# Performance work log

Measured on AMD Instinct MI355X. Metric: run time of the kernel, lower is better.

The kernel has to match this reference:

```python
import jax, jax.numpy as jnp
import numpy as np

NORM_EPS = 1e-6

B, C, H, W = 4, 256, 48, 48
CE = 512           # C * expansion_ratio
N_STATE = 16       # Mamba d_state
DT_RANK = 32       # Ce // 16


def setup_inputs() -> dict:
    key = jax.random.key(0)
    ks = jax.random.split(key, 12)
    s = 0.02
    inp = {
        "x": jax.random.normal(ks[0], (B, C, H, W), jnp.float32),
        "norm_w": jnp.ones((C,), jnp.float32),
        "norm_b": jnp.zeros((C,), jnp.float32),
        "w_ex": jax.random.normal(ks[1], (2 * CE, C), jnp.float32) * s,
        "b_ex": jnp.zeros((2 * CE,), jnp.float32),
        "w_proj": jax.random.normal(ks[2], (C, CE), jnp.float32) * s,
        "b_proj": jnp.zeros((C,), jnp.float32),
        "dw_kernel": jax.random.normal(ks[3], (3, 3, 1, CE), jnp.float32) * 0.1,  # HWIO depthwise
        "A_log": jnp.log(jnp.broadcast_to(jnp.arange(1, N_STATE + 1, dtype=jnp.float32), (CE, N_STATE))),
        "D": jnp.ones((CE,), jnp.float32),
        "W_xproj": jax.random.normal(ks[4], (DT_RANK + 2 * N_STATE, CE), jnp.float32) * s,
        "b_xproj": jnp.zeros((DT_RANK + 2 * N_STATE,), jnp.float32),
        "W_dt": jax.random.normal(ks[5], (CE, DT_RANK), jnp.float32) * s,
        "b_dt": jnp.full((CE,), -3.0, jnp.float32),  # softplus -> small positive dt
    }
    return inp


def _forward(x, norm_w, norm_b, w_ex, b_ex, w_proj, b_proj,
             dw_kernel, A_log, D, W_xproj, b_xproj, W_dt, b_dt):
    Bt, Cc, Hh, Ww = x.shape
    Ce = dw_kernel.shape[-1]
    Ns = A_log.shape[1]
    dt_rank = W_dt.shape[1]

    # NCHW -> NHWC, LayerNorm over C
    xp = jnp.transpose(x, (0, 2, 3, 1))
    mu = xp.mean(-1, keepdims=True)
    var = xp.var(-1, keepdims=True)
    xn = (xp - mu) * jax.lax.rsqrt(var + NORM_EPS) * norm_w + norm_b

    # expansion + split
    uv = xn @ w_ex.T + b_ex                       # [B,H,W,2Ce]
    u, v = jnp.split(uv, 2, axis=-1)
    gate = u * jax.nn.sigmoid(-u)                 # r_silu(u)
    g = u * jax.nn.sigmoid(u)                     # SiLU(u)

    # depthwise 3x3 conv (NHWC) + SiLU
    v = jax.lax.conv_general_dilated(
        v, dw_kernel, window_strides=(1, 1), padding='SAME',
        dimension_numbers=('NHWC', 'HWIO', 'NHWC'), feature_group_count=Ce)
    v = v * jax.nn.sigmoid(v)

    gate = v * gate                               # fuse gate before SSM

    # ---- Mamba selective scan over raster-flattened HW sequence ----
    L = Hh * Ww
    vs = v.reshape(Bt, L, Ce)                     # [B,L,Ce]
    dbc = vs @ W_xproj.T + b_xproj                # [B,L,dt_rank+2N]
    dt = dbc[..., :dt_rank]
    Bm = dbc[..., dt_rank:dt_rank + Ns]           # [B,L,N]
    Cm = dbc[..., dt_rank + Ns:]                  # [B,L,N]
    delta = jax.nn.softplus(dt @ W_dt.T + b_dt)   # [B,L,Ce]
    A = -jnp.exp(A_log)                           # [Ce,N], negative -> stable

    def step(h, inp):
        d_t, b_t, c_t, v_t = inp                  # [B,Ce],[B,N],[B,N],[B,Ce]
        dA = jnp.exp(d_t[..., None] * A)          # [B,Ce,N]
        h = h * dA + d_t[..., None] * b_t[:, None, :] * v_t[..., None]
        y = jnp.einsum('bcn,bn->bc', h, c_t) + D * v_t
        return h, y

    h0 = jnp.zeros((Bt, Ce, Ns), x.dtype)
    seq = (jnp.swapaxes(delta, 0, 1), jnp.swapaxes(Bm, 0, 1),
           jnp.swapaxes(Cm, 0, 1), jnp.swapaxes(vs, 0, 1))
    _, ys = jax.lax.scan(step, h0, seq)           # ys: [L,B,Ce]
    y = jnp.swapaxes(ys, 0, 1).reshape(Bt, Hh, Ww, Ce)

    out = (y * g + gate) @ w_proj.T + b_proj      # [B,H,W,C]
    return jnp.transpose(out, (0, 3, 1, 2))       # NCHW


def reference(x, norm_w, norm_b, w_ex, b_ex, w_proj, b_proj,
              dw_kernel, A_log, D, W_xproj, b_xproj, W_dt, b_dt):
    return _forward(x, norm_w, norm_b, w_ex, b_ex, w_proj, b_proj,
                    dw_kernel, A_log, D, W_xproj, b_xproj, W_dt, b_dt)
```

## Files before the change

### kernel.cpp

```cpp
#include <hip/hip_runtime.h>
#include <hip/hip_bf16.h>

#define B_   4
#define C_   256
#define HH   48
#define WW   48
#define L_   2304
#define BL   9216
#define CE_  512
#define NS   16
#define DTR  32
#define NCH  72
#define CHL  32

typedef __attribute__((ext_vector_type(8))) short s16x8;
typedef __attribute__((ext_vector_type(4))) float f32x4;

__device__ __forceinline__ ushort f2bf(float f) {
  union { float f; unsigned u; } v; v.f = f;
  unsigned r = v.u + 0x7fffu + ((v.u >> 16) & 1u);
  return (ushort)(r >> 16);
}
__device__ __forceinline__ float bf2f(ushort h) {
  union { unsigned u; float f; } v; v.u = ((unsigned)h) << 16;
  return v.f;
}

__global__ __launch_bounds__(256) void prep_cast_k(const float* __restrict__ w_ex,
                                                   const float* __restrict__ w_proj,
                                                   const float* __restrict__ b_xp,
                                                   const float* __restrict__ W_dt,
                                                   const float* __restrict__ b_dt,
                                                   ushort* __restrict__ w_ex_bf,
                                                   ushort* __restrict__ w_proj_bf,
                                                   float* __restrict__ bcat) {
  int idx = blockIdx.x * 256 + threadIdx.x;
  if (idx < 262144) {
    w_ex_bf[idx] = f2bf(w_ex[idx]);
  } else if (idx < 393216) {
    int i = idx - 262144; w_proj_bf[i] = f2bf(w_proj[i]);
  } else if (idx < 393792) {
    int n = idx - 393216;
    float s;
    if (n < 512) {
      s = b_dt[n];
      #pragma unroll
      for (int r = 0; r < 32; r++) s = fmaf(W_dt[n * 32 + r], b_xp[r], s);
    } else if (n < 544) {
      s = b_xp[32 + (n - 512)];
    } else s = 0.f;
    bcat[n] = s;
  }
}

__global__ __launch_bounds__(256) void wcat_k(const float* __restrict__ W_dt,
                                              const float* __restrict__ W_xp,
                                              ushort* __restrict__ wcat_bf) {
  int idx = blockIdx.x * 256 + threadIdx.x;
  int i = idx >> 9, j = idx & 511;
  float s = 0.f;
  if (i < 512) {
    #pragma unroll
    for (int r = 0; r < 32; r++) s = fmaf(W_dt[i * 32 + r], W_xp[r * 512 + j], s);
  } else if (i < 544) {
    s = W_xp[(i - 480) * 512 + j];
  }
  wcat_bf[idx] = f2bf(s);
}

__global__ __launch_bounds__(256) void ln_k(const float* __restrict__ x,
                                            const float* __restrict__ w,
                                            const float* __restrict__ bia,
                                            ushort* __restrict__ xn_bf) {
  __shared__ float xt[C_][17];
  __shared__ float ps[16][17], ps2[16][17];
  __shared__ float mu_s[16], r_s[16];
  int blk = blockIdx.x;
  int b = blk / 144, p0 = (blk - b * 144) * 16;
  int t = threadIdx.x;
  #pragma unroll
  for (int it = 0; it < 16; it++) {
    int i = it * 256 + t;
    int c = i >> 4, pj = i & 15;
    xt[c][pj] = x[((size_t)(b * C_ + c)) * L_ + p0 + pj];
  }
  __syncthreads();
  {
    int ci = t >> 4, pj = t & 15;
    float s = 0.f, s2 = 0.f;
    #pragma unroll
    for (int k = 0; k < 16; k++) {
      float v = xt[ci * 16 + k][pj];
      s += v; s2 += v * v;
    }
    ps[ci][pj] = s; ps2[ci][pj] = s2;
  }
  __syncthreads();
  if (t < 16) {
    float s = 0.f, s2 = 0.f;
    #pragma unroll
    for (int ci = 0; ci < 16; ci++) { s += ps[ci][t]; s2 += ps2[ci][t]; }
    float mu = s * (1.f / C_);
    float var = s2 * (1.f / C_) - mu * mu;
    mu_s[t] = mu; r_s[t] = rsqrtf(var + 1e-6f);
  }
  __syncthreads();
  float wr = w[t], br = bia[t];
  #pragma unroll
  for (int pj = 0; pj < 16; pj++) {
    float val = (xt[t][pj] - mu_s[pj]) * r_s[pj] * wr + br;
    xn_bf[((size_t)(b * L_ + p0 + pj)) * C_ + t] = f2bf(val);
  }
}

template<int TM, int TN, int WN, int FM, int FN, int K>
__device__ __forceinline__ void mfma_gemm(const ushort* __restrict__ A,
                                          const ushort* __restrict__ Bm,
                                          int m0, int n0,
                                          ushort* Als, ushort* Bls,
                                          f32x4 acc[FM][FN]) {
  const int t = threadIdx.x;
  const int lane = t & 63;
  const int wid = t >> 6;
  const int wm = wid / WN, wn = wid % WN;
  #pragma unroll
  for (int i = 0; i < FM; i++)
    #pragma unroll
    for (int j = 0; j < FN; j++) acc[i][j] = (f32x4){0.f, 0.f, 0.f, 0.f};

  for (int kt = 0; kt < K; kt += 32) {
    #pragma unroll
    for (int ch = t; ch < TM * 4; ch += 256) {
      int k8 = ch / TM, row = ch % TM;
      const ushort* g = A + (size_t)(m0 + row) * K + kt + k8 * 8;
      ushort* l = Als + (k8 * TM + row) * 8;
      __builtin_amdgcn_global_load_lds((const __attribute__((address_space(1))) void*)g,
                                       (__attribute__((address_space(3))) void*)l, 16, 0, 0);
    }
    #pragma unroll
    for (int ch = t; ch < TN * 4; ch += 256) {
      int k8 = ch / TN, row = ch % TN;
      const ushort* g = Bm + (size_t)(n0 + row) * K + kt + k8 * 8;
      ushort* l = Bls + (k8 * TN + row) * 8;
      __builtin_amdgcn_global_load_lds((const __attribute__((address_space(1))) void*)g,
                                       (__attribute__((address_space(3))) void*)l, 16, 0, 0);
    }
    __syncthreads();
    int k8 = lane >> 4, r = lane & 15;
    s16x8 a[FM], b[FN];
    #pragma unroll
    for (int i = 0; i < FM; i++)
      a[i] = *(const s16x8*)(Als + (k8 * TM + wm * FM * 16 + i * 16 + r) * 8);
    #pragma unroll
    for (int j = 0; j < FN; j++)
      b[j] = *(const s16x8*)(Bls + (k8 * TN + wn * FN * 16 + j * 16 + r) * 8);
    #pragma unroll
    for (int i = 0; i < FM; i++)
      #pragma unroll
      for (int j = 0; j < FN; j++)
        acc[i][j] = __builtin_amdgcn_mfma_f32_16x16x32_bf16(a[i], b[j], acc[i][j], 0, 0, 0);
    __syncthreads();
  }
}

__global__ __launch_bounds__(256) void gemm_expand_k(const ushort* __restrict__ xn,
                                                     const ushort* __restrict__ wex,
                                                     const float* __restrict__ b_ex,
                                                     ushort* __restrict__ u_bf,
                                                     ushort* __restrict__ v_bf) {
  __shared__ alignas(16) ushort Als[4 * 128 * 8];
  __shared__ alignas(16) ushort Bls[4 * 64 * 8];
  f32x4 acc[4][2];
  int m0 = blockIdx.y * 128, n0 = blockIdx.x * 64;
  mfma_gemm<128, 64, 2, 4, 2, 256>(xn, wex, m0, n0, Als, Bls, acc);
  int lane = threadIdx.x & 63, wid = threadIdx.x >> 6;
  int wm = wid >> 1, wn = wid & 1;
  int q4 = (lane >> 4) * 4, cix = lane & 15;
  ushort* base = (n0 < 512) ? u_bf : v_bf;
  int nbase = (n0 < 512) ? n0 : n0 - 512;
  #pragma unroll
  for (int j = 0; j < 2; j++) {
    int nc = nbase + wn * 32 + j * 16 + cix;
    float bias = b_ex[(n0 < 512 ? 0 : 512) + nc];
    #pragma unroll
    for (int i = 0; i < 4; i++) {
      int mr = m0 + wm * 64 + i * 16 + q4;
      #pragma unroll
      for (int q = 0; q < 4; q++)
        base[(size_t)(mr + q) * CE_ + nc] = f2bf(acc[i][j][q] + bias);
    }
  }
}

__global__ __launch_bounds__(256) void gemm_dbc_k(const ushort* __restrict__ vs,
                                                  const ushort* __restrict__ wcat,
                                                  const float* __restrict__ bcat,
                                                  float* __restrict__ delta,
                                                  float* __restrict__ bc) {
  __shared__ alignas(16) ushort Als[4 * 128 * 8];
  __shared__ alignas(16) ushort Bls[4 * 64 * 8];
  f32x4 acc[4][2];
  int m0 = blockIdx.y * 128, n0 = blockIdx.x * 64;
  mfma_gemm<128, 64, 2, 4, 2, 512>(vs, wcat, m0, n0, Als, Bls, acc);
  int lane = threadIdx.x & 63, wid = threadIdx.x >> 6;
  int wm = wid >> 1, wn = wid & 1;
  int q4 = (lane >> 4) * 4, cix = lane & 15;
  #pragma unroll
  for (int j = 0; j < 2; j++) {
    int nc = n0 + wn * 32 + j * 16 + cix;
    if (nc >= 544) continue;
    float bias = bcat[nc];
    #pragma unroll
    for (int i = 0; i < 4; i++) {
      int mr = m0 + wm * 64 + i * 16 + q4;
      #pragma unroll
      for (int q = 0; q < 4; q++) {
        float xv = acc[i][j][q] + bias;
        if (nc < 512)
          delta[(size_t)(mr + q) * CE_ + nc] =
              fmaxf(xv, 0.f) + __logf(1.f + __expf(-fabsf(xv)));
        else
          bc[(size_t)(mr + q) * 32 + (nc - 512)] = xv;
      }
    }
  }
}

__global__ __launch_bounds__(256) void gemm_proj_k(const ushort* __restrict__ z,
                                                   const ushort* __restrict__ wpr,
                                                   const float* __restrict__ b_proj,
                                                   float* __restrict__ out) {
  __shared__ alignas(16) ushort Als[4 * 64 * 8];
  __shared__ alignas(16) ushort Bls[4 * 64 * 8];
  f32x4 acc[2][2];
  int m0 = blockIdx.y * 64, n0 = blockIdx.x * 64;
  mfma_gemm<64, 64, 2, 2, 2, 512>(z, wpr, m0, n0, Als, Bls, acc);
  int lane = threadIdx.x & 63, wid = threadIdx.x >> 6;
  int wm = wid >> 1, wn = wid & 1;
  int q4 = (lane >> 4) * 4, cix = lane & 15;
  #pragma unroll
  for (int j = 0; j < 2; j++) {
    int nc = n0 + wn * 32 + j * 16 + cix;
    float bias = b_proj[nc];
    #pragma unroll
    for (int i = 0; i < 2; i++) {
      int pix = m0 + wm * 32 + i * 16 + q4;
      int b = pix / L_, p = pix - b * L_;
      float4 vv = make_float4(acc[i][j][0] + bias, acc[i][j][1] + bias,
                              acc[i][j][2] + bias, acc[i][j][3] + bias);
      *(float4*)&out[((size_t)(b * C_ + nc)) * L_ + p] = vv;
    }
  }
}

__global__ __launch_bounds__(256) void dwconv_k(const ushort* __restrict__ vraw,
                                                const float* __restrict__ kw,
                                                ushort* __restrict__ vs) {
  int p = blockIdx.x * 2 + (threadIdx.x >> 7);
  int b = p / L_, q = p - b * L_;
  int y = q / WW, x = q - y * WW;
  int c4 = (threadIdx.x & 127) * 4;
  float a0 = 0.f, a1 = 0.f, a2 = 0.f, a3 = 0.f;
  #pragma unroll
  for (int ky = 0; ky < 3; ky++) {
    int yy = y + ky - 1;
    if (yy < 0 || yy >= HH) continue;
    #pragma unroll
    for (int kx = 0; kx < 3; kx++) {
      int xx = x + kx - 1;
      if (xx < 0 || xx >= WW) continue;
      uint2 pv = *(const uint2*)(vraw + ((size_t)(b * L_ + yy * WW + xx)) * CE_ + c4);
      float4 kk = *(const float4*)(kw + (ky * 3 + kx) * CE_ + c4);
      a0 = fmaf(bf2f((ushort)(pv.x & 0xffff)), kk.x, a0);
      a1 = fmaf(bf2f((ushort)(pv.x >> 16)),    kk.y, a1);
      a2 = fmaf(bf2f((ushort)(pv.y & 0xffff)), kk.z, a2);
      a3 = fmaf(bf2f((ushort)(pv.y >> 16)),    kk.w, a3);
    }
  }
  float s0 = a0 / (1.f + __expf(-a0));
  float s1 = a1 / (1.f + __expf(-a1));
  float s2 = a2 / (1.f + __expf(-a2));
  float s3 = a3 / (1.f + __expf(-a3));
  uint2 outp;
  outp.x = (unsigned)f2bf(s0) | ((unsigned)f2bf(s1) << 16);
  outp.y = (unsigned)f2bf(s2) | ((unsigned)f2bf(s3) << 16);
  *(uint2*)(vs + (size_t)p * CE_ + c4) = outp;
}

__global__ __launch_bounds__(256) void scan1_k(const float* __restrict__ delta,
                                               const float* __restrict__ bc,
                                               const ushort* __restrict__ vs,
                                               const float* __restrict__ A_log,
                                               float* __restrict__ S,
                                               float* __restrict__ Dsum) {
  __shared__ float bt_s[CHL * NS];
  int b = blockIdx.z, ch = blockIdx.y;
  int c = blockIdx.x * 256 + threadIdx.x;
  int mbase = b * L_ + ch * CHL;
  for (int i = threadIdx.x; i < CHL * NS; i += 256)
    bt_s[i] = bc[(size_t)(mbase + (i >> 4)) * 32 + (i & 15)];
  __syncthreads();
  float Ac[NS], h[NS];
  #pragma unroll
  for (int n = 0; n < NS; n++) {
    Ac[n] = -__expf(A_log[c * NS + n]);
    h[n] = 0.f;
  }
  float dsum = 0.f;
  for (int t = 0; t < CHL; t++) {
    int m = mbase + t;
    float d  = delta[(size_t)m * CE_ + c];
    float vv = bf2f(vs[(size_t)m * CE_ + c]);
    float dv = d * vv;
    dsum += d;
    #pragma unroll
    for (int n = 0; n < NS; n++)
      h[n] = fmaf(h[n], __expf(d * Ac[n]), dv * bt_s[t * NS + n]);
  }
  size_t sidx = (size_t)(b * NCH + ch) * CE_ + c;
  #pragma unroll
  for (int n = 0; n < NS; n++) S[sidx * NS + n] = h[n];
  Dsum[sidx] = dsum;
}

__global__ __launch_bounds__(256) void scan2_k(const float* __restrict__ A_log,
                                               float* __restrict__ S,
                                               const float* __restrict__ Dsum) {
  int idx = blockIdx.x * 256 + threadIdx.x;
  int n = idx & 15, c = (idx >> 4) & (CE_ - 1), b = idx >> 13;
  float Ac = -__expf(A_log[c * NS + n]);
  float h = 0.f;
  for (int ch = 0; ch < NCH; ch++) {
    size_t sidx = (size_t)(b * NCH + ch) * CE_ + c;
    float sv = S[sidx * NS + n];
    float ds = Dsum[sidx];
    S[sidx * NS + n] = h;
    h = fmaf(h, __expf(Ac * ds), sv);
  }
}

__global__ __launch_bounds__(256) void scan3_k(const float* __restrict__ delta,
                                               const float* __restrict__ bc,
                                               const ushort* __restrict__ vs,
                                               const float* __restrict__ A_log,
                                               const float* __restrict__ Dv,
                                               const float* __restrict__ hstart,
                                               const ushort* __restrict__ u,
                                               ushort* __restrict__ z) {
  __shared__ float bc_s[CHL * 32];
  int b = blockIdx.z, ch = blockIdx.y;
  int c = blockIdx.x * 256 + threadIdx.x;
  int mbase = b * L_ + ch * CHL;
  for (int i = threadIdx.x; i < CHL * 32; i += 256)
    bc_s[i] = bc[(size_t)(mbase + (i >> 5)) * 32 + (i & 31)];
  __syncthreads();
  size_t sidx = (size_t)(b * NCH + ch) * CE_ + c;
  float Ac[NS], h[NS];
  #pragma unroll
  for (int n = 0; n < NS; n++) {
    Ac[n] = -__expf(A_log[c * NS + n]);
    h[n] = hstart[sidx * NS + n];
  }
  float Dc = Dv[c];
  for (int t = 0; t < CHL; t++) {
    int m = mbase + t;
    float d  = delta[(size_t)m * CE_ + c];
    float vv = bf2f(vs[(size_t)m * CE_ + c]);
    float dv = d * vv;
    float y = 0.f;
    #pragma unroll
    for (int n = 0; n < NS; n++) {
      h[n] = fmaf(h[n], __expf(d * Ac[n]), dv * bc_s[t * 32 + n]);
      y = fmaf(h[n], bc_s[t * 32 + 16 + n], y);
    }
    y = fmaf(Dc, vv, y);
    float uu = bf2f(u[(size_t)m * CE_ + c]);
    float s  = 1.f / (1.f + __expf(-uu));
    z[(size_t)m * CE_ + c] = f2bf(uu * (y * s + vv * (1.f - s)));
  }
}

extern "C" void kernel_launch(void* const* d_in, const int* in_sizes, int n_in,
                              void* d_out, int out_size, void* d_ws, size_t ws_size,
                              hipStream_t stream) {
  const float* x      = (const float*)d_in[0];
  const float* norm_w = (const float*)d_in[1];
  const float* norm_b = (const float*)d_in[2];
  const float* w_ex   = (const float*)d_in[3];
  const float* b_ex   = (const float*)d_in[4];
  const float* w_proj = (const float*)d_in[5];
  const float* b_proj = (const float*)d_in[6];
  const float* dw_k   = (const float*)d_in[7];
  const float* A_log  = (const float*)d_in[8];
  const float* Dv     = (const float*)d_in[9];
  const float* W_xp   = (const float*)d_in[10];
  const float* b_xp   = (const float*)d_in[11];
  const float* W_dt   = (const float*)d_in[12];
  const float* b_dt   = (const float*)d_in[13];
  float* out = (float*)d_out;

  char* wsb = (char*)d_ws;
  size_t off = 0;
  auto alloc = [&](size_t bytes) { void* p = wsb + off; off += (bytes + 255) & ~(size_t)255; return p; };
  ushort* u_bf    = (ushort*)alloc((size_t)BL * CE_ * 2);
  ushort* vraw_bf = (ushort*)alloc((size_t)BL * CE_ * 2);
  ushort* vs_bf   = (ushort*)alloc((size_t)BL * CE_ * 2);
  ushort* xn_bf   = (ushort*)alloc((size_t)BL * C_ * 2);
  float*  delta   = (float*)alloc((size_t)BL * CE_ * 4);
  float*  bc      = (float*)alloc((size_t)BL * 32 * 4);
  float*  S       = (float*)alloc((size_t)B_ * NCH * CE_ * NS * 4);
  float*  Dsum    = (float*)alloc((size_t)B_ * NCH * CE_ * 4);
  ushort* w_ex_bf = (ushort*)alloc((size_t)2 * CE_ * C_ * 2);
  ushort* w_pr_bf = (ushort*)alloc((size_t)C_ * CE_ * 2);
  ushort* wcat_bf = (ushort*)alloc((size_t)576 * CE_ * 2);
  float*  bcat    = (float*)alloc((size_t)576 * 4);
  ushort* z_bf = vraw_bf;

  prep_cast_k<<<1539, 256, 0, stream>>>(w_ex, w_proj, b_xp, W_dt, b_dt,
                                        w_ex_bf, w_pr_bf, bcat);
  wcat_k<<<1152, 256, 0, stream>>>(W_dt, W_xp, wcat_bf);
  ln_k<<<576, 256, 0, stream>>>(x, norm_w, norm_b, xn_bf);
  gemm_expand_k<<<dim3(16, 72), 256, 0, stream>>>(xn_bf, w_ex_bf, b_ex, u_bf, vraw_bf);
  dwconv_k<<<BL / 2, 256, 0, stream>>>(vraw_bf, dw_k, vs_bf);
  gemm_dbc_k<<<dim3(9, 72), 256, 0, stream>>>(vs_bf, wcat_bf, bcat, delta, bc);
  scan1_k<<<dim3(2, NCH, B_), 256, 0, stream>>>(delta, bc, vs_bf, A_log, S, Dsum);
  scan2_k<<<128, 256, 0, stream>>>(A_log, S, Dsum);
  scan3_k<<<dim3(2, NCH, B_), 256, 0, stream>>>(delta, bc, vs_bf, A_log, Dv, S, u_bf, z_bf);
  gemm_proj_k<<<dim3(4, 144), 256, 0, stream>>>(z_bf, w_pr_bf, b_proj, out);
}
```

Before: 243.2 us.

## Double-buffer GEMM LDS loads, stage epilogues through LDS, merge prep kernels

The shared MFMA GEMM helper now double-buffers its LDS tiles, issuing the next k-slice's global-to-LDS loads before computing on the current one. The expand GEMM grows to a 128x128 tile and writes bf16 through an LDS staging tile so rows are stored as wide 16-byte writes. The projection GEMM transposes its output through LDS for coalesced NCHW float4 stores. The two weight-prep kernels are merged into one launch, LayerNorm writes vectorized bf16 rows, and dwconv uses cheaper bf16 unpacking. In exchange, the larger LDS footprint and tiles may lower occupancy, and the expand grid gets fewer blocks.

```diff
diff --git a/kernel.cpp b/kernel.cpp
--- a/kernel.cpp
+++ b/kernel.cpp
@@ -25,22 +25,41 @@
   union { unsigned u; float f; } v; v.u = ((unsigned)h) << 16;
   return v.f;
 }
-
-__global__ __launch_bounds__(256) void prep_cast_k(const float* __restrict__ w_ex,
-                                                   const float* __restrict__ w_proj,
-                                                   const float* __restrict__ b_xp,
-                                                   const float* __restrict__ W_dt,
-                                                   const float* __restrict__ b_dt,
-                                                   ushort* __restrict__ w_ex_bf,
-                                                   ushort* __restrict__ w_proj_bf,
-                                                   float* __restrict__ bcat) {
+__device__ __forceinline__ float lo_f(unsigned u) {
+  union { unsigned u; float f; } v; v.u = u << 16; return v.f;
+}
+__device__ __forceinline__ float hi_f(unsigned u) {
+  union { unsigned u; float f; } v; v.u = u & 0xffff0000u; return v.f;
+}
+
+__global__ __launch_bounds__(256) void prep_k(const float* __restrict__ w_ex,
+                                              const float* __restrict__ w_proj,
+                                              const float* __restrict__ W_xp,
+                                              const float* __restrict__ b_xp,
+                                              const float* __restrict__ W_dt,
+                                              const float* __restrict__ b_dt,
+                                              ushort* __restrict__ w_ex_bf,
+                                              ushort* __restrict__ w_proj_bf,
+                                              ushort* __restrict__ wcat_bf,
+                                              float* __restrict__ bcat) {
   int idx = blockIdx.x * 256 + threadIdx.x;
   if (idx < 262144) {
     w_ex_bf[idx] = f2bf(w_ex[idx]);
   } else if (idx < 393216) {
     int i = idx - 262144; w_proj_bf[i] = f2bf(w_proj[i]);
-  } else if (idx < 393792) {
-    int n = idx - 393216;
+  } else if (idx < 688128) {
+    int i2 = idx - 393216;
+    int i = i2 >> 9, j = i2 & 511;
+    float s = 0.f;
+    if (i < 512) {
+      #pragma unroll
+      for (int r = 0; r < 32; r++) s = fmaf(W_dt[i * 32 + r], W_xp[r * 512 + j], s);
+    } else if (i < 544) {
+      s = W_xp[(i - 480) * 512 + j];
+    }
+    wcat_bf[i2] = f2bf(s);
+  } else if (idx < 688704) {
+    int n = idx - 688128;
     float s;
     if (n < 512) {
       s = b_dt[n];
@@ -51,21 +70,6 @@
     } else s = 0.f;
     bcat[n] = s;
   }
-}
-
-__global__ __launch_bounds__(256) void wcat_k(const float* __restrict__ W_dt,
-                                              const float* __restrict__ W_xp,
-                                              ushort* __restrict__ wcat_bf) {
-  int idx = blockIdx.x * 256 + threadIdx.x;
-  int i = idx >> 9, j = idx & 511;
-  float s = 0.f;
-  if (i < 512) {
-    #pragma unroll
-    for (int r = 0; r < 32; r++) s = fmaf(W_dt[i * 32 + r], W_xp[r * 512 + j], s);
-  } else if (i < 544) {
-    s = W_xp[(i - 480) * 512 + j];
-  }
-  wcat_bf[idx] = f2bf(s);
 }
 
 __global__ __launch_bounds__(256) void ln_k(const float* __restrict__ x,
@@ -75,9 +79,11 @@
   __shared__ float xt[C_][17];
   __shared__ float ps[16][17], ps2[16][17];
   __shared__ float mu_s[16], r_s[16];
+  __shared__ float w_s[C_], b_s[C_];
   int blk = blockIdx.x;
   int b = blk / 144, p0 = (blk - b * 144) * 16;
   int t = threadIdx.x;
+  w_s[t] = w[t]; b_s[t] = bia[t];
   #pragma unroll
   for (int it = 0; it < 16; it++) {
     int i = it * 256 + t;
@@ -105,55 +111,77 @@
     mu_s[t] = mu; r_s[t] = rsqrtf(var + 1e-6f);
   }
   __syncthreads();
-  float wr = w[t], br = bia[t];
-  #pragma unroll
-  for (int pj = 0; pj < 16; pj++) {
-    float val = (xt[t][pj] - mu_s[pj]) * r_s[pj] * wr + br;
-    xn_bf[((size_t)(b * L_ + p0 + pj)) * C_ + t] = f2bf(val);
-  }
+  int pj = t & 15, c0 = (t >> 4) * 16;
+  float mu = mu_s[pj], r = r_s[pj];
+  s16x8 v0, v1;
+  #pragma unroll
+  for (int k = 0; k < 8; k++) {
+    int c = c0 + k;
+    v0[k] = (short)f2bf((xt[c][pj] - mu) * r * w_s[c] + b_s[c]);
+  }
+  #pragma unroll
+  for (int k = 0; k < 8; k++) {
+    int c = c0 + 8 + k;
+    v1[k] = (short)f2bf((xt[c][pj] - mu) * r * w_s[c] + b_s[c]);
+  }
+  ushort* dst = xn_bf + ((size_t)(b * L_ + p0 + pj)) * C_ + c0;
+  *(s16x8*)dst = v0;
+  *(s16x8*)(dst + 8) = v1;
 }
 
 template<int TM, int TN, int WN, int FM, int FN, int K>
 __device__ __forceinline__ void mfma_gemm(const ushort* __restrict__ A,
                                           const ushort* __restrict__ Bm,
-                                          int m0, int n0,
-                                          ushort* Als, ushort* Bls,
+                                          int m0, int n0, ushort* sh,
                                           f32x4 acc[FM][FN]) {
   const int t = threadIdx.x;
   const int lane = t & 63;
   const int wid = t >> 6;
   const int wm = wid / WN, wn = wid % WN;
+  constexpr int ASZ = TM * 32, BSZ = TN * 32;
   #pragma unroll
   for (int i = 0; i < FM; i++)
     #pragma unroll
     for (int j = 0; j < FN; j++) acc[i][j] = (f32x4){0.f, 0.f, 0.f, 0.f};
 
-  for (int kt = 0; kt < K; kt += 32) {
+  auto stage = [&](int kt, int buf) {
+    ushort* Ad = sh + buf * (ASZ + BSZ);
+    ushort* Bd = Ad + ASZ;
     #pragma unroll
     for (int ch = t; ch < TM * 4; ch += 256) {
       int k8 = ch / TM, row = ch % TM;
       const ushort* g = A + (size_t)(m0 + row) * K + kt + k8 * 8;
-      ushort* l = Als + (k8 * TM + row) * 8;
-      __builtin_amdgcn_global_load_lds((const __attribute__((address_space(1))) void*)g,
-                                       (__attribute__((address_space(3))) void*)l, 16, 0, 0);
+      __builtin_amdgcn_global_load_lds(
+          (const __attribute__((address_space(1))) void*)g,
+          (__attribute__((address_space(3))) void*)(Ad + (k8 * TM + row) * 8), 16, 0, 0);
     }
     #pragma unroll
     for (int ch = t; ch < TN * 4; ch += 256) {
       int k8 = ch / TN, row = ch % TN;
       const ushort* g = Bm + (size_t)(n0 + row) * K + kt + k8 * 8;
-      ushort* l = Bls + (k8 * TN + row) * 8;
-      __builtin_amdgcn_global_load_lds((const __attribute__((address_space(1))) void*)g,
-                                       (__attribute__((address_space(3))) void*)l, 16, 0, 0);
-    }
-    __syncthreads();
-    int k8 = lane >> 4, r = lane & 15;
+      __builtin_amdgcn_global_load_lds(
+          (const __attribute__((address_space(1))) void*)g,
+          (__attribute__((address_space(3))) void*)(Bd + (k8 * TN + row) * 8), 16, 0, 0);
+    }
+  };
+
+  stage(0, 0);
+  __syncthreads();
+  constexpr int NK = K / 32;
+  const int k8 = lane >> 4, r = lane & 15;
+  #pragma unroll
+  for (int kt = 0; kt < NK; kt++) {
+    const int cur = kt & 1;
+    if (kt + 1 < NK) stage((kt + 1) * 32, cur ^ 1);
+    const ushort* Ab = sh + cur * (ASZ + BSZ);
+    const ushort* Bb = Ab + ASZ;
     s16x8 a[FM], b[FN];
     #pragma unroll
     for (int i = 0; i < FM; i++)
-      a[i] = *(const s16x8*)(Als + (k8 * TM + wm * FM * 16 + i * 16 + r) * 8);
+      a[i] = *(const s16x8*)(Ab + (k8 * TM + wm * FM * 16 + i * 16 + r) * 8);
     #pragma unroll
     for (int j = 0; j < FN; j++)
-      b[j] = *(const s16x8*)(Bls + (k8 * TN + wn * FN * 16 + j * 16 + r) * 8);
+      b[j] = *(const s16x8*)(Bb + (k8 * TN + wn * FN * 16 + j * 16 + r) * 8);
     #pragma unroll
     for (int i = 0; i < FM; i++)
       #pragma unroll
@@ -168,28 +196,35 @@
                                                      const float* __restrict__ b_ex,
                                                      ushort* __restrict__ u_bf,
                                                      ushort* __restrict__ v_bf) {
-  __shared__ alignas(16) ushort Als[4 * 128 * 8];
-  __shared__ alignas(16) ushort Bls[4 * 64 * 8];
-  f32x4 acc[4][2];
-  int m0 = blockIdx.y * 128, n0 = blockIdx.x * 64;
-  mfma_gemm<128, 64, 2, 4, 2, 256>(xn, wex, m0, n0, Als, Bls, acc);
+  __shared__ __align__(16) ushort sh[128 * 136];
+  f32x4 acc[4][4];
+  int m0 = blockIdx.y * 128, n0 = blockIdx.x * 128;
+  mfma_gemm<128, 128, 2, 4, 4, 256>(xn, wex, m0, n0, sh, acc);
   int lane = threadIdx.x & 63, wid = threadIdx.x >> 6;
   int wm = wid >> 1, wn = wid & 1;
   int q4 = (lane >> 4) * 4, cix = lane & 15;
+  const int ST = 136;
+  #pragma unroll
+  for (int j = 0; j < 4; j++) {
+    int ncl = wn * 64 + j * 16 + cix;
+    float bias = b_ex[n0 + ncl];
+    #pragma unroll
+    for (int i = 0; i < 4; i++) {
+      int ml = wm * 64 + i * 16 + q4;
+      #pragma unroll
+      for (int q = 0; q < 4; q++)
+        sh[(ml + q) * ST + ncl] = f2bf(acc[i][j][q] + bias);
+    }
+  }
+  __syncthreads();
   ushort* base = (n0 < 512) ? u_bf : v_bf;
-  int nbase = (n0 < 512) ? n0 : n0 - 512;
-  #pragma unroll
-  for (int j = 0; j < 2; j++) {
-    int nc = nbase + wn * 32 + j * 16 + cix;
-    float bias = b_ex[(n0 < 512 ? 0 : 512) + nc];
-    #pragma unroll
-    for (int i = 0; i < 4; i++) {
-      int mr = m0 + wm * 64 + i * 16 + q4;
-      #pragma unroll
-      for (int q = 0; q < 4; q++)
-        base[(size_t)(mr + q) * CE_ + nc] = f2bf(acc[i][j][q] + bias);
-    }
-  }
+  int nb = (n0 < 512) ? n0 : n0 - 512;
+  int ml = threadIdx.x >> 1, nc0 = (threadIdx.x & 1) * 64;
+  ushort* dst = base + (size_t)(m0 + ml) * CE_ + nb + nc0;
+  const ushort* srcp = sh + ml * ST + nc0;
+  #pragma unroll
+  for (int k = 0; k < 8; k++)
+    *(s16x8*)(dst + k * 8) = *(const s16x8*)(srcp + k * 8);
 }
 
 __global__ __launch_bounds__(256) void gemm_dbc_k(const ushort* __restrict__ vs,
@@ -197,11 +232,10 @@
                                                   const float* __restrict__ bcat,
                                                   float* __restrict__ delta,
                                                   float* __restrict__ bc) {
-  __shared__ alignas(16) ushort Als[4 * 128 * 8];
-  __shared__ alignas(16) ushort Bls[4 * 64 * 8];
+  __shared__ __align__(16) ushort sh[2 * (128 * 32 + 64 * 32)];
   f32x4 acc[4][2];
   int m0 = blockIdx.y * 128, n0 = blockIdx.x * 64;
-  mfma_gemm<128, 64, 2, 4, 2, 512>(vs, wcat, m0, n0, Als, Bls, acc);
+  mfma_gemm<128, 64, 2, 4, 2, 512>(vs, wcat, m0, n0, sh, acc);
   int lane = threadIdx.x & 63, wid = threadIdx.x >> 6;
   int wm = wid >> 1, wn = wid & 1;
   int q4 = (lane >> 4) * 4, cix = lane & 15;
@@ -230,26 +264,35 @@
                                                    const ushort* __restrict__ wpr,
                                                    const float* __restrict__ b_proj,
                                                    float* __restrict__ out) {
-  __shared__ alignas(16) ushort Als[4 * 64 * 8];
-  __shared__ alignas(16) ushort Bls[4 * 64 * 8];
+  __shared__ __align__(16) ushort sh[2 * (64 * 32 + 64 * 32)];
+  __shared__ float Cs[64][65];
   f32x4 acc[2][2];
   int m0 = blockIdx.y * 64, n0 = blockIdx.x * 64;
-  mfma_gemm<64, 64, 2, 2, 2, 512>(z, wpr, m0, n0, Als, Bls, acc);
-  int lane = threadIdx.x & 63, wid = threadIdx.x >> 6;
+  mfma_gemm<64, 64, 2, 2, 2, 512>(z, wpr, m0, n0, sh, acc);
+  int t = threadIdx.x;
+  int lane = t & 63, wid = t >> 6;
   int wm = wid >> 1, wn = wid & 1;
   int q4 = (lane >> 4) * 4, cix = lane & 15;
   #pragma unroll
-  for (int j = 0; j < 2; j++) {
-    int nc = n0 + wn * 32 + j * 16 + cix;
-    float bias = b_proj[nc];
-    #pragma unroll
-    for (int i = 0; i < 2; i++) {
-      int pix = m0 + wm * 32 + i * 16 + q4;
-      int b = pix / L_, p = pix - b * L_;
-      float4 vv = make_float4(acc[i][j][0] + bias, acc[i][j][1] + bias,
-                              acc[i][j][2] + bias, acc[i][j][3] + bias);
-      *(float4*)&out[((size_t)(b * C_ + nc)) * L_ + p] = vv;
-    }
+  for (int j = 0; j < 2; j++)
+    #pragma unroll
+    for (int i = 0; i < 2; i++)
+      #pragma unroll
+      for (int q = 0; q < 4; q++)
+        Cs[wm * 32 + i * 16 + q4 + q][wn * 32 + j * 16 + cix] = acc[i][j][q];
+  __syncthreads();
+  int nc_l = t >> 2, p4 = (t & 3) * 16;
+  float bias = b_proj[n0 + nc_l];
+  int pix0 = m0 + p4;
+  int bb = pix0 / L_, p = pix0 - bb * L_;
+  float* dst = out + ((size_t)(bb * C_ + n0 + nc_l)) * L_ + p;
+  #pragma unroll
+  for (int k = 0; k < 4; k++) {
+    float4 vv = make_float4(Cs[p4 + k * 4 + 0][nc_l] + bias,
+                            Cs[p4 + k * 4 + 1][nc_l] + bias,
+                            Cs[p4 + k * 4 + 2][nc_l] + bias,
+                            Cs[p4 + k * 4 + 3][nc_l] + bias);
+    *(float4*)(dst + k * 4) = vv;
   }
 }
 
@@ -271,10 +314,10 @@
       if (xx < 0 || xx >= WW) continue;
       uint2 pv = *(const uint2*)(vraw + ((size_t)(b * L_ + yy * WW + xx)) * CE_ + c4);
       float4 kk = *(const float4*)(kw + (ky * 3 + kx) * CE_ + c4);
-      a0 = fmaf(bf2f((ushort)(pv.x & 0xffff)), kk.x, a0);
-      a1 = fmaf(bf2f((ushort)(pv.x >> 16)),    kk.y, a1);
-      a2 = fmaf(bf2f((ushort)(pv.y & 0xffff)), kk.z, a2);
-      a3 = fmaf(bf2f((ushort)(pv.y >> 16)),    kk.w, a3);
+      a0 = fmaf(lo_f(pv.x), kk.x, a0);
+      a1 = fmaf(hi_f(pv.x), kk.y, a1);
+      a2 = fmaf(lo_f(pv.y), kk.z, a2);
+      a3 = fmaf(hi_f(pv.y), kk.w, a3);
     }
   }
   float s0 = a0 / (1.f + __expf(-a0));
@@ -416,11 +459,10 @@
   float*  bcat    = (float*)alloc((size_t)576 * 4);
   ushort* z_bf = vraw_bf;
 
-  prep_cast_k<<<1539, 256, 0, stream>>>(w_ex, w_proj, b_xp, W_dt, b_dt,
-                                        w_ex_bf, w_pr_bf, bcat);
-  wcat_k<<<1152, 256, 0, stream>>>(W_dt, W_xp, wcat_bf);
+  prep_k<<<2691, 256, 0, stream>>>(w_ex, w_proj, W_xp, b_xp, W_dt, b_dt,
+                                   w_ex_bf, w_pr_bf, wcat_bf, bcat);
   ln_k<<<576, 256, 0, stream>>>(x, norm_w, norm_b, xn_bf);
-  gemm_expand_k<<<dim3(16, 72), 256, 0, stream>>>(xn_bf, w_ex_bf, b_ex, u_bf, vraw_bf);
+  gemm_expand_k<<<dim3(8, 72), 256, 0, stream>>>(xn_bf, w_ex_bf, b_ex, u_bf, vraw_bf);
   dwconv_k<<<BL / 2, 256, 0, stream>>>(vraw_bf, dw_k, vs_bf);
   gemm_dbc_k<<<dim3(9, 72), 256, 0, stream>>>(vs_bf, wcat_bf, bcat, delta, bc);
   scan1_k<<<dim3(2, NCH, B_), 256, 0, stream>>>(delta, bc, vs_bf, A_log, S, Dsum);
```

Measured after the change: 245.6 us. Within noise of the previous version (+1.0%).
